# Optimization experiments

Measured on AMD Instinct MI355X. Metric: run time of the kernel, lower is better.

## Reference

```python
import jax, jax.numpy as jnp
import numpy as np

NEG_SLOPE = 0.2


def setup_inputs() -> dict:
    key = jax.random.key(0)
    ks = jax.random.split(key, 12)
    Nm, Na, E, Din, H, D = 50000, 50000, 400000, 128, 8, 32
    return {
        "master_feats": jax.random.normal(ks[0], (Nm, Din), jnp.float32),
        "attn_feats0": jax.random.normal(ks[1], (Na, Din), jnp.float32),
        "attn_feats1": jax.random.normal(ks[2], (Na, Din), jnp.float32),
        "src0": jax.random.randint(ks[3], (E,), 0, Na, jnp.int32),
        "dst0": jax.random.randint(ks[4], (E,), 0, Nm, jnp.int32),
        "src1": jax.random.randint(ks[5], (E,), 0, Na, jnp.int32),
        "dst1": jax.random.randint(ks[6], (E,), 0, Nm, jnp.int32),
        "W_master": jax.random.normal(ks[7], (Din, H * D), jnp.float32) * 0.08,
        "W0": jax.random.normal(ks[8], (Din, H * D), jnp.float32) * 0.08,
        "W1": jax.random.normal(ks[9], (Din, H * D), jnp.float32) * 0.08,
        "attn_l": jax.random.normal(ks[10], (H, D), jnp.float32) * 0.1,
        "attn_r": jax.random.normal(ks[11], (H, D), jnp.float32) * 0.1,
    }


def reference(master_feats, attn_feats0, attn_feats1, src0, dst0, src1, dst1,
              W_master, W0, W1, attn_l, attn_r):
    Nm = master_feats.shape[0]
    H, D = attn_l.shape

    # Per-node-type linear projections (no bias) + attention logits.
    ft_m = (master_feats @ W_master).reshape(Nm, H, D)        # [Nm,H,D]
    er = jnp.einsum("nhd,hd->nh", ft_m, attn_r)               # [Nm,H]

    def proj(feats, W):
        ft = (feats @ W).reshape(feats.shape[0], H, D)
        el = jnp.einsum("nhd,hd->nh", ft, attn_l)
        return ft, el

    ft0, el0 = proj(attn_feats0, W0)
    ft1, el1 = proj(attn_feats1, W1)

    lrelu = lambda x: jnp.where(x >= 0, x, NEG_SLOPE * x)
    e0 = lrelu(el0[src0] + er[dst0])                          # [E0,H]
    e1 = lrelu(el1[src1] + er[dst1])                          # [E1,H]

    # Heterograph edge softmax: normalize over ALL incoming edges of each
    # master node, regardless of source node type (subtract dst-max for
    # stability; mathematically identical to the conditional path in source).
    dst = jnp.concatenate([dst0, dst1])
    e = jnp.concatenate([e0, e1], axis=0)                     # [E0+E1,H]
    emax = jax.ops.segment_max(e, dst, num_segments=Nm)
    emax = jnp.where(jnp.isfinite(emax), emax, 0.0)           # nodes w/o edges
    ee = jnp.exp(e - emax[dst])
    esum = jax.ops.segment_sum(ee, dst, num_segments=Nm)
    a = ee / esum[dst]                                        # [E0+E1,H]

    # u_mul_e + sum aggregation onto master nodes.
    E0 = src0.shape[0]
    msg = jnp.concatenate(
        [ft0[src0] * a[:E0, :, None], ft1[src1] * a[E0:, :, None]], axis=0
    )                                                         # [E,H,D]
    rst = jax.ops.segment_sum(msg, dst, num_segments=Nm)      # [Nm,H,D]
    return rst
```

## Files before the change

### kernel.cpp

```cpp
#include <hip/hip_runtime.h>
#include <cstdint>
#include <cstddef>

#define NEG_SLOPE 0.2f

typedef __attribute__((ext_vector_type(8))) short short8;
typedef __attribute__((ext_vector_type(4))) float f32x4;

static __device__ __forceinline__ unsigned short f2bf(float x) {
  uint32_t u = __float_as_uint(x);
  uint32_t r = (u + 0x7FFFu + ((u >> 16) & 1u)) >> 16;
  return (unsigned short)r;
}
static __device__ __forceinline__ float bf2f(unsigned short b) {
  return __uint_as_float(((uint32_t)b) << 16);
}

__global__ void wt_kernel(const float* __restrict__ W0, const float* __restrict__ W1,
                          const float* __restrict__ W2,
                          unsigned short* __restrict__ T0, unsigned short* __restrict__ T1,
                          unsigned short* __restrict__ T2) {
  const float* W = (blockIdx.y == 0) ? W0 : (blockIdx.y == 1) ? W1 : W2;
  unsigned short* T = (blockIdx.y == 0) ? T0 : (blockIdx.y == 1) ? T1 : T2;
  int c = blockIdx.x * 2 + (threadIdx.x >> 7);
  int k = threadIdx.x & 127;
  T[c * 128 + k] = f2bf(W[k * 256 + c]);
}

__global__ __launch_bounds__(256)
void proj_mfma_kernel(const float* __restrict__ fm, const float* __restrict__ fa0,
                      const float* __restrict__ fa1,
                      const unsigned short* __restrict__ Wtm,
                      const unsigned short* __restrict__ Wt0,
                      const unsigned short* __restrict__ Wt1,
                      const float* __restrict__ attn_l, const float* __restrict__ attn_r,
                      int Nm, int Na0, int Na1,
                      unsigned short* __restrict__ ft_all, float* __restrict__ el_all,
                      float* __restrict__ er) {
  const int z = blockIdx.z;
  const float* feats = (z == 0) ? fm : (z == 1) ? fa0 : fa1;
  const unsigned short* Wt = (z == 0) ? Wtm : (z == 1) ? Wt0 : Wt1;
  const float* av = (z == 0) ? attn_r : attn_l;
  const int N = (z == 0) ? Nm : (z == 1) ? Na0 : Na1;
  unsigned short* ft_out = (z == 0) ? nullptr
                         : (z == 1) ? ft_all : ft_all + (size_t)Na0 * 256;
  float* el_out = (z == 0) ? er : (z == 1) ? el_all : el_all + (size_t)Na0 * 8;

  const int rb = blockIdx.x * 64;
  if (rb >= N) return;

  __shared__ unsigned short As[64 * 128];
  const int t = threadIdx.x;
  const int wid = t >> 6, lane = t & 63;
  const int l15 = lane & 15, l4 = lane >> 4;
  const int cbw = wid * 64;
  const int head0 = cbw >> 5;

  short8 bf[4][4];
  #pragma unroll
  for (int nf = 0; nf < 4; ++nf) {
    const unsigned short* wp = &Wt[(size_t)(cbw + nf * 16 + l15) * 128];
    #pragma unroll
    for (int kb = 0; kb < 4; ++kb)
      bf[kb][nf] = *(const short8*)(wp + kb * 32 + l4 * 8);
  }

  #pragma unroll
  for (int it = 0; it < 8; ++it) {
    int i = it * 256 + t;
    int r = i >> 5, kc = (i & 31) << 2;
    float4 f = make_float4(0.f, 0.f, 0.f, 0.f);
    if (rb + r < N) f = *(const float4*)(&feats[(size_t)(rb + r) * 128 + kc]);
    ushort4 u;
    u.x = f2bf(f.x); u.y = f2bf(f.y); u.z = f2bf(f.z); u.w = f2bf(f.w);
    uint32_t byte = ((uint32_t)(r * 256 + kc * 2)) ^ ((uint32_t)((r & 7) << 4));
    *(ushort4*)((char*)As + byte) = u;
  }
  __syncthreads();

  f32x4 acc[4][4];
  #pragma unroll
  for (int a = 0; a < 4; ++a)
    #pragma unroll
    for (int b = 0; b < 4; ++b)
      acc[a][b] = (f32x4){0.f, 0.f, 0.f, 0.f};

  #pragma unroll
  for (int kb = 0; kb < 4; ++kb) {
    short8 af[4];
    #pragma unroll
    for (int mf = 0; mf < 4; ++mf) {
      int row = mf * 16 + l15;
      uint32_t byte = ((uint32_t)(row * 256 + kb * 64 + l4 * 16)) ^ ((uint32_t)((row & 7) << 4));
      af[mf] = *(const short8*)((const char*)As + byte);
    }
    #pragma unroll
    for (int mf = 0; mf < 4; ++mf)
      #pragma unroll
      for (int nf = 0; nf < 4; ++nf)
        acc[mf][nf] = __builtin_amdgcn_mfma_f32_16x16x32_bf16(
            bf[kb][nf], af[mf], acc[mf][nf], 0, 0, 0);
  }

  float avf[4][4];
  #pragma unroll
  for (int nf = 0; nf < 4; ++nf)
    #pragma unroll
    for (int reg = 0; reg < 4; ++reg)
      avf[nf][reg] = av[(head0 + (nf >> 1)) * 32 + (nf & 1) * 16 + l4 * 4 + reg];

  #pragma unroll
  for (int mf = 0; mf < 4; ++mf) {
    int node = rb + mf * 16 + l15;
    bool ok = node < N;
    if (ft_out != nullptr && ok) {
      size_t base = (size_t)node * 256 + cbw + l4 * 4;
      #pragma unroll
      for (int nf = 0; nf < 4; ++nf) {
        ushort4 u;
        u.x = f2bf(acc[mf][nf][0]); u.y = f2bf(acc[mf][nf][1]);
        u.z = f2bf(acc[mf][nf][2]); u.w = f2bf(acc[mf][nf][3]);
        *(ushort4*)(&ft_out[base + nf * 16]) = u;
      }
    }
    #pragma unroll
    for (int hh = 0; hh < 2; ++hh) {
      float p = 0.f;
      #pragma unroll
      for (int reg = 0; reg < 4; ++reg) {
        p = fmaf(acc[mf][2 * hh][reg], avf[2 * hh][reg], p);
        p = fmaf(acc[mf][2 * hh + 1][reg], avf[2 * hh + 1][reg], p);
      }
      p += __shfl_xor(p, 16);
      p += __shfl_xor(p, 32);
      if (ok && l4 == 0)
        el_out[(size_t)node * 8 + head0 + hh] = p;
    }
  }
}

__global__ void count_deg_kernel(const int* __restrict__ dst0, int E0,
                                 const int* __restrict__ dst1, int E1,
                                 int* __restrict__ deg) {
  int E = E0 + E1;
  for (int i = blockIdx.x * blockDim.x + threadIdx.x; i < E;
       i += gridDim.x * blockDim.x) {
    int d = (i < E0) ? dst0[i] : dst1[i - E0];
    atomicAdd(&deg[d], 1);
  }
}

__global__ __launch_bounds__(1024)
void block_reduce_kernel(const int* __restrict__ deg, int* __restrict__ partial, int n) {
  __shared__ int wsum[16];
  const int t = threadIdx.x;
  int idx = blockIdx.x * 1024 + t;
  int v = (idx < n) ? deg[idx] : 0;
  #pragma unroll
  for (int off = 1; off < 64; off <<= 1) v += __shfl_xor(v, off);
  if ((t & 63) == 0) wsum[t >> 6] = v;
  __syncthreads();
  if (t < 16) {
    int x = wsum[t];
    #pragma unroll
    for (int off = 1; off < 16; off <<= 1) x += __shfl_xor(x, off);
    if (t == 0) partial[blockIdx.x] = x;
  }
}

__global__ __launch_bounds__(64)
void partial_scan_kernel(const int* __restrict__ partial, int* __restrict__ base,
                         int nb, int* __restrict__ offs, int n) {
  const int t = threadIdx.x;
  int v = (t < nb) ? partial[t] : 0;
  int incl = v;
  #pragma unroll
  for (int off = 1; off < 64; off <<= 1) {
    int x = __shfl_up(incl, off);
    if (t >= off) incl += x;
  }
  if (t < nb) base[t] = incl - v;
  if (t == nb - 1) offs[n] = incl;
}

__global__ __launch_bounds__(1024)
void apply_scan_kernel(const int* __restrict__ deg, const int* __restrict__ base,
                       int* __restrict__ offs, int* __restrict__ cursor, int n) {
  __shared__ int wsum[16];
  const int t = threadIdx.x;
  const int idx = blockIdx.x * 1024 + t;
  int v = (idx < n) ? deg[idx] : 0;
  const int lane = t & 63, w = t >> 6;
  int incl = v;
  #pragma unroll
  for (int off = 1; off < 64; off <<= 1) {
    int x = __shfl_up(incl, off);
    if (lane >= off) incl += x;
  }
  if (lane == 63) wsum[w] = incl;
  __syncthreads();
  if (t < 16) {
    int x = wsum[t];
    #pragma unroll
    for (int off = 1; off < 16; off <<= 1) {
      int y = __shfl_up(x, off);
      if (t >= off) x += y;
    }
    wsum[t] = x;
  }
  __syncthreads();
  int excl = base[blockIdx.x] + ((w > 0) ? wsum[w - 1] : 0) + incl - v;
  if (idx < n) {
    offs[idx] = excl;
    cursor[idx] = excl;
  }
}

__global__ void scatter_kernel(const int* __restrict__ src0, const int* __restrict__ dst0, int E0,
                               const int* __restrict__ src1, const int* __restrict__ dst1, int E1,
                               int* __restrict__ cursor, char* __restrict__ recs,
                               const float* __restrict__ el, const float* __restrict__ er,
                               int Na0) {
  int E = E0 + E1;
  for (int i = blockIdx.x * blockDim.x + threadIdx.x; i < E;
       i += gridDim.x * blockDim.x) {
    int s, d;
    if (i < E0) { s = src0[i]; d = dst0[i]; }
    else        { s = src1[i - E0] + Na0; d = dst1[i - E0]; }
    int pos = atomicAdd(&cursor[d], 1);

    const float* elp = &el[(size_t)s * 8];
    const float* erp = &er[(size_t)d * 8];
    float4 ea = *(const float4*)elp, eb = *(const float4*)(elp + 4);
    float4 ra = *(const float4*)erp, rb = *(const float4*)(erp + 4);
    float w[8];
    w[0] = ea.x + ra.x; w[1] = ea.y + ra.y; w[2] = ea.z + ra.z; w[3] = ea.w + ra.w;
    w[4] = eb.x + rb.x; w[5] = eb.y + rb.y; w[6] = eb.z + rb.z; w[7] = eb.w + rb.w;
    uint32_t pk[4];
    #pragma unroll
    for (int q = 0; q < 4; ++q) {
      float v0 = w[2 * q], v1 = w[2 * q + 1];
      v0 = fmaxf(v0, NEG_SLOPE * v0);
      v1 = fmaxf(v1, NEG_SLOPE * v1);
      uint32_t b0 = f2bf(__expf(v0)), b1 = f2bf(__expf(v1));
      pk[q] = b0 | (b1 << 16);
    }
    char* rp = recs + ((size_t)(uint32_t)pos << 5);
    *(uint4*)rp = make_uint4((uint32_t)s, pk[0], pk[1], pk[2]);
    *(uint32_t*)(rp + 16) = pk[3];
  }
}

__global__ __launch_bounds__(256)
void aggregate_kernel(const int* __restrict__ offs, const char* __restrict__ recs,
                      const unsigned short* __restrict__ ft,
                      float* __restrict__ rst, int Nm) {
  int gid = blockIdx.x * blockDim.x + threadIdx.x;
  int n = gid >> 6;
  int lane = threadIdx.x & 63;
  if (n >= Nm) return;
  const int nu = __builtin_amdgcn_readfirstlane(n);
  const int beg = offs[nu], end = offs[nu + 1];
  const int h = lane >> 3;
  const char* ftl = (const char*)ft + lane * 8;
  float o0 = 0.f, o1 = 0.f, o2 = 0.f, o3 = 0.f;
  float sw = 0.f;

  #pragma unroll 4
  for (int i = beg; i < end; ++i) {
    const uint32_t* rp = (const uint32_t*)(recs + ((size_t)(uint32_t)i << 5));
    uint32_t sct = rp[0];
    uint32_t d0 = rp[1], d1 = rp[2], d2 = rp[3], d3 = rp[4];
    uint2 g = *(const uint2*)(ftl + ((size_t)sct << 9));
    uint32_t wa = (h & 2) ? d1 : d0;
    uint32_t wb = (h & 2) ? d3 : d2;
    uint32_t wsl = (h & 4) ? wb : wa;
    float w = __uint_as_float((h & 1) ? (wsl & 0xffff0000u) : (wsl << 16));
    sw += w;
    o0 = fmaf(w, __uint_as_float(g.x << 16), o0);
    o1 = fmaf(w, __uint_as_float(g.x & 0xffff0000u), o1);
    o2 = fmaf(w, __uint_as_float(g.y << 16), o2);
    o3 = fmaf(w, __uint_as_float(g.y & 0xffff0000u), o3);
  }

  if (beg < end) {
    float inv = 1.0f / sw;
    o0 *= inv; o1 *= inv; o2 *= inv; o3 *= inv;
  }
  *(float4*)(&rst[(size_t)n * 256 + lane * 4]) = make_float4(o0, o1, o2, o3);
}

extern "C" void kernel_launch(void* const* d_in, const int* in_sizes, int n_in,
                              void* d_out, int out_size, void* d_ws, size_t ws_size,
                              hipStream_t stream) {
  const float* master = (const float*)d_in[0];
  const float* af0    = (const float*)d_in[1];
  const float* af1    = (const float*)d_in[2];
  const int*   src0   = (const int*)d_in[3];
  const int*   dst0   = (const int*)d_in[4];
  const int*   src1   = (const int*)d_in[5];
  const int*   dst1   = (const int*)d_in[6];
  const float* Wm     = (const float*)d_in[7];
  const float* W0     = (const float*)d_in[8];
  const float* W1     = (const float*)d_in[9];
  const float* attn_l = (const float*)d_in[10];
  const float* attn_r = (const float*)d_in[11];

  const int Nm  = in_sizes[0] / 128;
  const int Na0 = in_sizes[1] / 128;
  const int Na1 = in_sizes[2] / 128;
  const int E0  = in_sizes[3];
  const int E1  = in_sizes[5];
  float* rst = (float*)d_out;

  char* ws = (char*)d_ws;
  size_t off = 0;
  auto alloc = [&](size_t b) -> char* {
    char* p = ws + off;
    off += (b + 511) & ~(size_t)511;
    return p;
  };
  unsigned short* ft = (unsigned short*)alloc((size_t)(Na0 + Na1) * 256 * sizeof(unsigned short));
  float* el = (float*)alloc((size_t)(Na0 + Na1) * 8 * sizeof(float));
  float* er = (float*)alloc((size_t)Nm * 8 * sizeof(float));
  unsigned short* Wtm = (unsigned short*)alloc(256 * 128 * sizeof(unsigned short));
  unsigned short* Wt0 = (unsigned short*)alloc(256 * 128 * sizeof(unsigned short));
  unsigned short* Wt1 = (unsigned short*)alloc(256 * 128 * sizeof(unsigned short));
  int* deg     = (int*)alloc((size_t)Nm * sizeof(int));
  int* offs    = (int*)alloc((size_t)(Nm + 1) * sizeof(int));
  int* cursor  = (int*)alloc((size_t)Nm * sizeof(int));
  int* partial = (int*)alloc(64 * sizeof(int));
  int* pbase   = (int*)alloc(64 * sizeof(int));
  char* recs   = alloc((size_t)(E0 + E1) * 32);

  wt_kernel<<<dim3(128, 3), 256, 0, stream>>>(Wm, W0, W1, Wtm, Wt0, Wt1);

  int Nmax = Nm > Na0 ? Nm : Na0; if (Na1 > Nmax) Nmax = Na1;
  const int mb = (Nmax + 63) / 64;
  proj_mfma_kernel<<<dim3(mb, 1, 3), 256, 0, stream>>>(
      master, af0, af1, Wtm, Wt0, Wt1, attn_l, attn_r,
      Nm, Na0, Na1, ft, el, er);

  hipMemsetAsync(deg, 0, (size_t)Nm * sizeof(int), stream);
  count_deg_kernel<<<1024, 256, 0, stream>>>(dst0, E0, dst1, E1, deg);
  const int nb = (Nm + 1023) / 1024;
  block_reduce_kernel<<<nb, 1024, 0, stream>>>(deg, partial, Nm);
  partial_scan_kernel<<<1, 64, 0, stream>>>(partial, pbase, nb, offs, Nm);
  apply_scan_kernel<<<nb, 1024, 0, stream>>>(deg, pbase, offs, cursor, Nm);
  scatter_kernel<<<1024, 256, 0, stream>>>(src0, dst0, E0, src1, dst1, E1,
                                           cursor, recs, el, er, Na0);

  aggregate_kernel<<<(Nm + 3) / 4, 256, 0, stream>>>(offs, recs, ft, rst, Nm);
}
```

Measured before the change: 206.8 us.

## Move edge logit computation from scatter into aggregation, store only source index

The scatter kernel now writes only the 4-byte source index per edge into CSR slots instead of a 32-byte record holding packed bf16 exp-logits. The aggregate kernel loads el for the source per head, adds the per-node er (loaded once), and applies leaky-relu and exp inline. This cuts scatter write traffic and record read traffic by roughly 8x. In exchange it adds a gathered el load per edge and per-lane exp in aggregation, and it keeps fp32 weights rather than bf16-rounded ones.

New measurement: 236.3 us. 1.14x slower.

```diff
diff --git a/kernel.cpp b/kernel.cpp
--- a/kernel.cpp
+++ b/kernel.cpp
@@ -218,9 +218,7 @@
 
 __global__ void scatter_kernel(const int* __restrict__ src0, const int* __restrict__ dst0, int E0,
                                const int* __restrict__ src1, const int* __restrict__ dst1, int E1,
-                               int* __restrict__ cursor, char* __restrict__ recs,
-                               const float* __restrict__ el, const float* __restrict__ er,
-                               int Na0) {
+                               int* __restrict__ cursor, int* __restrict__ slots, int Na0) {
   int E = E0 + E1;
   for (int i = blockIdx.x * blockDim.x + threadIdx.x; i < E;
        i += gridDim.x * blockDim.x) {
@@ -228,31 +226,13 @@
     if (i < E0) { s = src0[i]; d = dst0[i]; }
     else        { s = src1[i - E0] + Na0; d = dst1[i - E0]; }
     int pos = atomicAdd(&cursor[d], 1);
-
-    const float* elp = &el[(size_t)s * 8];
-    const float* erp = &er[(size_t)d * 8];
-    float4 ea = *(const float4*)elp, eb = *(const float4*)(elp + 4);
-    float4 ra = *(const float4*)erp, rb = *(const float4*)(erp + 4);
-    float w[8];
-    w[0] = ea.x + ra.x; w[1] = ea.y + ra.y; w[2] = ea.z + ra.z; w[3] = ea.w + ra.w;
-    w[4] = eb.x + rb.x; w[5] = eb.y + rb.y; w[6] = eb.z + rb.z; w[7] = eb.w + rb.w;
-    uint32_t pk[4];
-    #pragma unroll
-    for (int q = 0; q < 4; ++q) {
-      float v0 = w[2 * q], v1 = w[2 * q + 1];
-      v0 = fmaxf(v0, NEG_SLOPE * v0);
-      v1 = fmaxf(v1, NEG_SLOPE * v1);
-      uint32_t b0 = f2bf(__expf(v0)), b1 = f2bf(__expf(v1));
-      pk[q] = b0 | (b1 << 16);
-    }
-    char* rp = recs + ((size_t)(uint32_t)pos << 5);
-    *(uint4*)rp = make_uint4((uint32_t)s, pk[0], pk[1], pk[2]);
-    *(uint32_t*)(rp + 16) = pk[3];
+    slots[pos] = s;
   }
 }
 
 __global__ __launch_bounds__(256)
-void aggregate_kernel(const int* __restrict__ offs, const char* __restrict__ recs,
+void aggregate_kernel(const int* __restrict__ offs, const int* __restrict__ slots,
+                      const float* __restrict__ el, const float* __restrict__ er,
                       const unsigned short* __restrict__ ft,
                       float* __restrict__ rst, int Nm) {
   int gid = blockIdx.x * blockDim.x + threadIdx.x;
@@ -263,19 +243,18 @@
   const int beg = offs[nu], end = offs[nu + 1];
   const int h = lane >> 3;
   const char* ftl = (const char*)ft + lane * 8;
+  const float ern = er[(size_t)nu * 8 + h];
   float o0 = 0.f, o1 = 0.f, o2 = 0.f, o3 = 0.f;
   float sw = 0.f;
 
   #pragma unroll 4
   for (int i = beg; i < end; ++i) {
-    const uint32_t* rp = (const uint32_t*)(recs + ((size_t)(uint32_t)i << 5));
-    uint32_t sct = rp[0];
-    uint32_t d0 = rp[1], d1 = rp[2], d2 = rp[3], d3 = rp[4];
-    uint2 g = *(const uint2*)(ftl + ((size_t)sct << 9));
-    uint32_t wa = (h & 2) ? d1 : d0;
-    uint32_t wb = (h & 2) ? d3 : d2;
-    uint32_t wsl = (h & 4) ? wb : wa;
-    float w = __uint_as_float((h & 1) ? (wsl & 0xffff0000u) : (wsl << 16));
+    int s = slots[i];
+    float ev = el[(size_t)(uint32_t)s * 8 + h];
+    uint2 g = *(const uint2*)(ftl + ((size_t)(uint32_t)s << 9));
+    float v = ev + ern;
+    v = fmaxf(v, NEG_SLOPE * v);
+    float w = __expf(v);
     sw += w;
     o0 = fmaf(w, __uint_as_float(g.x << 16), o0);
     o1 = fmaf(w, __uint_as_float(g.x & 0xffff0000u), o1);
@@ -331,7 +310,7 @@
   int* cursor  = (int*)alloc((size_t)Nm * sizeof(int));
   int* partial = (int*)alloc(64 * sizeof(int));
   int* pbase   = (int*)alloc(64 * sizeof(int));
-  char* recs   = alloc((size_t)(E0 + E1) * 32);
+  int* slots   = (int*)alloc((size_t)(E0 + E1) * sizeof(int));
 
   wt_kernel<<<dim3(128, 3), 256, 0, stream>>>(Wm, W0, W1, Wtm, Wt0, Wt1);
 
@@ -348,7 +327,7 @@
   partial_scan_kernel<<<1, 64, 0, stream>>>(partial, pbase, nb, offs, Nm);
   apply_scan_kernel<<<nb, 1024, 0, stream>>>(deg, pbase, offs, cursor, Nm);
   scatter_kernel<<<1024, 256, 0, stream>>>(src0, dst0, E0, src1, dst1, E1,
-                                           cursor, recs, el, er, Na0);
-
-  aggregate_kernel<<<(Nm + 3) / 4, 256, 0, stream>>>(offs, recs, ft, rst, Nm);
-}
+                                           cursor, slots, Na0);
+
+  aggregate_kernel<<<(Nm + 3) / 4, 256, 0, stream>>>(offs, slots, el, er, ft, rst, Nm);
+}
```
